# Optimization experiments

Hardware: AMD Instinct MI355X
Metric: run time of the kernel (lower is better)

Reference implementation:

```python
import jax, jax.numpy as jnp
import numpy as np

N, E, G = 100000, 1600000, 1024
F_IN, D, C = 1, 32, 10

def _lin(key, fin, fout):
    return jax.random.normal(key, (fin, fout), jnp.float32) / np.sqrt(fin)

def setup_inputs() -> dict:
    key = jax.random.key(0)
    ks = jax.random.split(key, 32)
    inp = {}
    inp['x'] = jax.random.normal(ks[0], (N, F_IN), jnp.float32)
    inp['edge_index'] = jax.random.randint(ks[1], (2, E), 0, N)
    inp['batch'] = jnp.sort(jax.random.randint(ks[2], (N,), 0, G))
    inp['num_graphs'] = G
    # conv1: ResGatedGraphConv(F_IN -> D)
    inp['c1_Wk'] = _lin(ks[3], F_IN, D); inp['c1_bk'] = jnp.zeros((D,), jnp.float32)
    inp['c1_Wq'] = _lin(ks[4], F_IN, D); inp['c1_bq'] = jnp.zeros((D,), jnp.float32)
    inp['c1_Wv'] = _lin(ks[5], F_IN, D); inp['c1_bv'] = jnp.zeros((D,), jnp.float32)
    inp['c1_Wskip'] = _lin(ks[6], F_IN, D); inp['c1_b'] = jnp.zeros((D,), jnp.float32)
    # conv2: FiLMConv(D -> D), num_relations=1
    inp['c2_Wlin'] = _lin(ks[7], D, D)
    inp['c2_Wfilm'] = _lin(ks[8], D, 2 * D); inp['c2_bfilm'] = jnp.zeros((2 * D,), jnp.float32)
    inp['c2_Wls'] = _lin(ks[9], D, D)
    inp['c2_Wfs'] = _lin(ks[10], D, 2 * D)
    # conv3: ResGatedGraphConv(D -> D)
    inp['c3_Wk'] = _lin(ks[11], D, D); inp['c3_bk'] = jnp.zeros((D,), jnp.float32)
    inp['c3_Wq'] = _lin(ks[12], D, D); inp['c3_bq'] = jnp.zeros((D,), jnp.float32)
    inp['c3_Wv'] = _lin(ks[13], D, D); inp['c3_bv'] = jnp.zeros((D,), jnp.float32)
    inp['c3_Wskip'] = _lin(ks[14], D, D); inp['c3_b'] = jnp.zeros((D,), jnp.float32)
    # final classifier
    inp['lin_W'] = _lin(ks[15], D, C); inp['lin_b'] = jnp.zeros((C,), jnp.float32)
    return inp

def _res_gated(x, src, dst, Wk, bk, Wq, bq, Wv, bv, Wskip, b):
    # out_i = sum_{j->i} sigmoid(k_i + q_j) * v_j + W_skip x_i + b
    k = x @ Wk + bk
    q = x @ Wq + bq
    v = x @ Wv + bv
    msg = jax.nn.sigmoid(k[dst] + q[src]) * v[src]  # [E, D]
    agg = jax.ops.segment_sum(msg, dst, num_segments=x.shape[0])
    return agg + x @ Wskip + b

def _film(x, src, dst, Wlin, Wfilm, bfilm, Wls, Wfs):
    # skip path: relu(gamma_skip * (W_skip x) + beta_skip)
    bg_s = x @ Wfs                       # [N, 2D]
    beta_s, gamma_s = jnp.split(bg_s, 2, axis=-1)
    out = jax.nn.relu(gamma_s * (x @ Wls) + beta_s)
    # message path: relu(gamma_i * (W x_j) + beta_i), mean aggregation
    bg = x @ Wfilm + bfilm
    beta, gamma = jnp.split(bg, 2, axis=-1)
    xl = x @ Wlin
    msg = jax.nn.relu(gamma[dst] * xl[src] + beta[dst])  # [E, D]
    sums = jax.ops.segment_sum(msg, dst, num_segments=x.shape[0])
    cnt = jax.ops.segment_sum(jnp.ones((dst.shape[0], 1), x.dtype), dst, num_segments=x.shape[0])
    return out + sums / jnp.maximum(cnt, 1.0)

def reference(x, edge_index, batch, num_graphs,
              c1_Wk, c1_bk, c1_Wq, c1_bq, c1_Wv, c1_bv, c1_Wskip, c1_b,
              c2_Wlin, c2_Wfilm, c2_bfilm, c2_Wls, c2_Wfs,
              c3_Wk, c3_bk, c3_Wq, c3_bq, c3_Wv, c3_bv, c3_Wskip, c3_b,
              lin_W, lin_b):
    src, dst = edge_index[0], edge_index[1]
    h = _res_gated(x, src, dst, c1_Wk, c1_bk, c1_Wq, c1_bq, c1_Wv, c1_bv, c1_Wskip, c1_b)
    h = jax.nn.relu(h)
    h = _film(h, src, dst, c2_Wlin, c2_Wfilm, c2_bfilm, c2_Wls, c2_Wfs)
    h = jax.nn.relu(h)
    h = _res_gated(h, src, dst, c3_Wk, c3_bk, c3_Wq, c3_bq, c3_Wv, c3_bv, c3_Wskip, c3_b)
    # global mean pool over graphs
    sums = jax.ops.segment_sum(h, batch, num_segments=num_graphs)
    cnt = jax.ops.segment_sum(jnp.ones((h.shape[0], 1), h.dtype), batch, num_segments=num_graphs)
    g = sums / jnp.maximum(cnt, 1.0)
    # dropout is identity in eval mode
    return g @ lin_W + lin_b
```

## Files before the change

kernel.cpp:

```cpp
#include <hip/hip_runtime.h>

#define N_NODES 100000
#define N_EDGES 1600000
#define N_GRAPH 1024
#define NB      196
#define BCAP    10240
#define PEPT    16

typedef unsigned short u16;
typedef unsigned int   u32;

__device__ __forceinline__ u16 f2bf(float f) {
    u32 u = __float_as_uint(f);
    u += 0x7FFFu + ((u >> 16) & 1u);
    return (u16)(u >> 16);
}
__device__ __forceinline__ float bf2f(u16 h) { return __uint_as_float(((u32)h) << 16); }
__device__ __forceinline__ float rcpf(float x) { return __builtin_amdgcn_rcpf(x); }

__global__ __launch_bounds__(256) void k_partition(const int* __restrict__ ei,
                                                   int* __restrict__ gcnt,
                                                   int* __restrict__ bucketed)
{
    __shared__ int lcnt[NB], gbase[NB], lcur[NB];
    int t = threadIdx.x;
    for (int i = t; i < NB; i += 256) { lcnt[i] = 0; lcur[i] = 0; }
    __syncthreads();

    int ebase = blockIdx.x * (256 * PEPT);
    int pk[PEPT], bk[PEPT];
#pragma unroll
    for (int r = 0; r < PEPT; r++) {
        int e = ebase + r * 256 + t;
        if (e < N_EDGES) {
            int d = ei[N_EDGES + e];
            int s = ei[e];
            int b = d >> 9;
            bk[r] = b;
            pk[r] = ((d & 511) << 17) | s;
            atomicAdd(&lcnt[b], 1);
        } else bk[r] = -1;
    }
    __syncthreads();
    for (int i = t; i < NB; i += 256) gbase[i] = atomicAdd(&gcnt[i], lcnt[i]);
    __syncthreads();
#pragma unroll
    for (int r = 0; r < PEPT; r++) {
        if (bk[r] >= 0) {
            int b = bk[r];
            int pos = gbase[b] + atomicAdd(&lcur[b], 1);
            bucketed[b * BCAP + pos] = pk[r];
        }
    }
}

__global__ __launch_bounds__(256) void k_bscan(const int* __restrict__ gcnt,
                                               int* __restrict__ base)
{
    __shared__ int s[256];
    int t = threadIdx.x;
    int v = (t < NB) ? gcnt[t] : 0;
    s[t] = v;
    __syncthreads();
#pragma unroll
    for (int off = 1; off < 256; off <<= 1) {
        int u = (t >= off) ? s[t - off] : 0;
        __syncthreads();
        s[t] += u;
        __syncthreads();
    }
    base[t] = s[t] - v;
}

__global__ __launch_bounds__(512) void k_place(const int* __restrict__ bucketed,
                                               const int* __restrict__ gcnt,
                                               const int* __restrict__ base,
                                               int* __restrict__ csr,
                                               int* __restrict__ starts,
                                               int* __restrict__ cnt)
{
    __shared__ int scnt[512], sexc[512], scur[512];
    int b = blockIdx.x, t = threadIdx.x;
    int ecnt = gcnt[b];
    int ebase = base[b];
    const int* bp = bucketed + b * BCAP;

    scnt[t] = 0; scur[t] = 0;
    __syncthreads();
    for (int e = t; e < ecnt; e += 512) atomicAdd(&scnt[bp[e] >> 17], 1);
    __syncthreads();
    int v = scnt[t];
    sexc[t] = v;
    __syncthreads();
#pragma unroll
    for (int off = 1; off < 512; off <<= 1) {
        int u = (t >= off) ? sexc[t - off] : 0;
        __syncthreads();
        sexc[t] += u;
        __syncthreads();
    }
    int excl = sexc[t] - v;
    __syncthreads();
    sexc[t] = excl;
    __syncthreads();

    int node = b * 512 + t;
    if (node < N_NODES) { starts[node] = ebase + excl; cnt[node] = v; }

    for (int e = t; e < ecnt; e += 512) {
        int p = bp[e];
        int ld = p >> 17;
        int pos = ebase + sexc[ld] + atomicAdd(&scur[ld], 1);
        csr[pos] = p & 0x1FFFF;
    }
}

__global__ __launch_bounds__(256) void k_gstart(const int* __restrict__ batch,
                                                int* __restrict__ gstart)
{
    int g = blockIdx.x * 256 + threadIdx.x;
    if (g > N_GRAPH) return;
    int lo = 0, hi = N_NODES;
    while (lo < hi) {
        int mid = (lo + hi) >> 1;
        if (batch[mid] < g) lo = mid + 1; else hi = mid;
    }
    gstart[g] = lo;
}

#define EDGE1(XS, ACC) {                                                     \
    ACC.x += fmaf(XS, wv.x, bv4.x) *                                         \
             rcpf(fmaf(ek.x, __expf(-fmaf(XS, wq.x, bq4.x)), 1.0f));         \
    ACC.y += fmaf(XS, wv.y, bv4.y) *                                         \
             rcpf(fmaf(ek.y, __expf(-fmaf(XS, wq.y, bq4.y)), 1.0f));         \
    ACC.z += fmaf(XS, wv.z, bv4.z) *                                         \
             rcpf(fmaf(ek.z, __expf(-fmaf(XS, wq.z, bq4.z)), 1.0f));         \
    ACC.w += fmaf(XS, wv.w, bv4.w) *                                         \
             rcpf(fmaf(ek.w, __expf(-fmaf(XS, wq.w, bq4.w)), 1.0f)); }

__global__ __launch_bounds__(256) void k_gath1(
    const float* __restrict__ x, const int* __restrict__ csr_src,
    const int* __restrict__ starts, const int* __restrict__ cnt,
    const float* __restrict__ Wk, const float* __restrict__ bk,
    const float* __restrict__ Wq, const float* __restrict__ bq,
    const float* __restrict__ Wv, const float* __restrict__ bv,
    const float* __restrict__ Wskip, const float* __restrict__ b,
    float* __restrict__ h1)
{
    int tid = blockIdx.x * 256 + threadIdx.x;
    int i = tid >> 3, l = tid & 7;

    float xd = x[i];
    float4 wk = ((const float4*)Wk)[l], bk4 = ((const float4*)bk)[l];
    float4 wq = ((const float4*)Wq)[l], bq4 = ((const float4*)bq)[l];
    float4 wv = ((const float4*)Wv)[l], bv4 = ((const float4*)bv)[l];
    float4 ek;
    ek.x = __expf(-fmaf(xd, wk.x, bk4.x));
    ek.y = __expf(-fmaf(xd, wk.y, bk4.y));
    ek.z = __expf(-fmaf(xd, wk.z, bk4.z));
    ek.w = __expf(-fmaf(xd, wk.w, bk4.w));

    int base = starts[i], deg = cnt[i];
    float4 a0 = make_float4(0.f, 0.f, 0.f, 0.f);
    float4 a1 = make_float4(0.f, 0.f, 0.f, 0.f);
    int e = 0;
    for (; e + 1 < deg; e += 2) {
        int s0 = csr_src[base + e];
        int s1 = csr_src[base + e + 1];
        float x0 = x[s0], x1 = x[s1];
        EDGE1(x0, a0) EDGE1(x1, a1)
    }
    if (e < deg) {
        float x0 = x[csr_src[base + e]];
        EDGE1(x0, a0)
    }
    float4 ws4 = ((const float4*)Wskip)[l];
    float4 bb4 = ((const float4*)b)[l];
    float4 o = make_float4(a0.x + a1.x + fmaf(xd, ws4.x, bb4.x),
                           a0.y + a1.y + fmaf(xd, ws4.y, bb4.y),
                           a0.z + a1.z + fmaf(xd, ws4.z, bb4.z),
                           a0.w + a1.w + fmaf(xd, ws4.w, bb4.w));
    ((float4*)(h1 + (size_t)i * 32))[l] = o;
}

__device__ __forceinline__ float4 dot4(const float* __restrict__ h,
                                       const float* __restrict__ Wcol, int stride)
{
    float4 a = make_float4(0.f, 0.f, 0.f, 0.f);
#pragma unroll
    for (int k = 0; k < 32; k++) {
        float4 w = *(const float4*)(Wcol + k * stride);
        float hk = h[k];
        a.x = fmaf(hk, w.x, a.x);
        a.y = fmaf(hk, w.y, a.y);
        a.z = fmaf(hk, w.z, a.z);
        a.w = fmaf(hk, w.w, a.w);
    }
    return a;
}

__global__ __launch_bounds__(256) void k_node2(
    const float* __restrict__ h1,
    const float* __restrict__ Wlin, const float* __restrict__ Wfilm,
    const float* __restrict__ bfilm, const float* __restrict__ Wls,
    const float* __restrict__ Wfs,
    u16* __restrict__ skip2b, u16* __restrict__ bg2b, u16* __restrict__ xlb)
{
    __shared__ float sWlin[1024], sWfilm[2048], sWls[1024], sWfs[2048];
    int t = threadIdx.x;
    for (int idx = t; idx < 1024; idx += 256) sWlin[idx] = Wlin[idx];
    for (int idx = t; idx < 2048; idx += 256) sWfilm[idx] = Wfilm[idx];
    for (int idx = t; idx < 1024; idx += 256) sWls[idx] = Wls[idx];
    for (int idx = t; idx < 2048; idx += 256) sWfs[idx] = Wfs[idx];
    __syncthreads();

    int tid = blockIdx.x * 256 + t;
    int i = tid >> 3, l = tid & 7;

    float h[32];
    const float4* hp = (const float4*)(h1 + (size_t)i * 32);
#pragma unroll
    for (int j = 0; j < 8; j++) {
        float4 v = hp[j];
        h[4 * j + 0] = fmaxf(v.x, 0.f);
        h[4 * j + 1] = fmaxf(v.y, 0.f);
        h[4 * j + 2] = fmaxf(v.z, 0.f);
        h[4 * j + 3] = fmaxf(v.w, 0.f);
    }

    float4 bs = dot4(h, sWfs + l * 4, 64);
    float4 gs = dot4(h, sWfs + 32 + l * 4, 64);
    float4 ls = dot4(h, sWls + l * 4, 32);
    ushort4 sku;
    sku.x = f2bf(fmaxf(fmaf(gs.x, ls.x, bs.x), 0.f));
    sku.y = f2bf(fmaxf(fmaf(gs.y, ls.y, bs.y), 0.f));
    sku.z = f2bf(fmaxf(fmaf(gs.z, ls.z, bs.z), 0.f));
    sku.w = f2bf(fmaxf(fmaf(gs.w, ls.w, bs.w), 0.f));
    ((ushort4*)skip2b)[(size_t)i * 8 + l] = sku;

    float4 bf0 = ((const float4*)bfilm)[l * 2];
    float4 bf1 = ((const float4*)bfilm)[l * 2 + 1];
    float4 f0 = dot4(h, sWfilm + l * 8, 64);
    float4 f1 = dot4(h, sWfilm + l * 8 + 4, 64);
    f0.x += bf0.x; f0.y += bf0.y; f0.z += bf0.z; f0.w += bf0.w;
    f1.x += bf1.x; f1.y += bf1.y; f1.z += bf1.z; f1.w += bf1.w;
    uint4 pk;
    pk.x = (u32)f2bf(f0.x) | ((u32)f2bf(f0.y) << 16);
    pk.y = (u32)f2bf(f0.z) | ((u32)f2bf(f0.w) << 16);
    pk.z = (u32)f2bf(f1.x) | ((u32)f2bf(f1.y) << 16);
    pk.w = (u32)f2bf(f1.z) | ((u32)f2bf(f1.w) << 16);
    ((uint4*)bg2b)[(size_t)i * 8 + l] = pk;

    float4 xo = dot4(h, sWlin + l * 4, 32);
    ushort4 xp;
    xp.x = f2bf(xo.x); xp.y = f2bf(xo.y); xp.z = f2bf(xo.z); xp.w = f2bf(xo.w);
    ((ushort4*)xlb)[(size_t)i * 8 + l] = xp;
}

#define EDGE_ACC2(U, ACC)                                   \
    ACC.x += fmaxf(fmaf(ga.x, bf2f(U.x), be.x), 0.f);       \
    ACC.y += fmaxf(fmaf(ga.y, bf2f(U.y), be.y), 0.f);       \
    ACC.z += fmaxf(fmaf(ga.z, bf2f(U.z), be.z), 0.f);       \
    ACC.w += fmaxf(fmaf(ga.w, bf2f(U.w), be.w), 0.f);

__global__ __launch_bounds__(256) void k_gath2(
    const int* __restrict__ csr_src, const int* __restrict__ starts,
    const int* __restrict__ cnt,
    const u16* __restrict__ bg2b, const u16* __restrict__ xlb,
    const u16* __restrict__ skip2b, float* __restrict__ h2)
{
    int tid = blockIdx.x * 256 + threadIdx.x;
    int i = tid >> 3, l = tid & 7;

    const u16* row = bg2b + (size_t)i * 64;
    ushort4 beu = *(const ushort4*)(row + l * 4);
    ushort4 gau = *(const ushort4*)(row + 32 + l * 4);
    float4 be = make_float4(bf2f(beu.x), bf2f(beu.y), bf2f(beu.z), bf2f(beu.w));
    float4 ga = make_float4(bf2f(gau.x), bf2f(gau.y), bf2f(gau.z), bf2f(gau.w));

    int base = starts[i], deg = cnt[i];
    const ushort4* xp = (const ushort4*)xlb;
    float4 a0 = make_float4(0.f, 0.f, 0.f, 0.f);
    float4 a1 = make_float4(0.f, 0.f, 0.f, 0.f);
    int e = 0;
    for (; e + 3 < deg; e += 4) {
        int s0 = csr_src[base + e];
        int s1 = csr_src[base + e + 1];
        int s2 = csr_src[base + e + 2];
        int s3 = csr_src[base + e + 3];
        ushort4 u0 = xp[(size_t)s0 * 8 + l];
        ushort4 u1 = xp[(size_t)s1 * 8 + l];
        ushort4 u2 = xp[(size_t)s2 * 8 + l];
        ushort4 u3 = xp[(size_t)s3 * 8 + l];
        EDGE_ACC2(u0, a0) EDGE_ACC2(u1, a1) EDGE_ACC2(u2, a0) EDGE_ACC2(u3, a1)
    }
    for (; e < deg; e++) {
        ushort4 u0 = xp[(size_t)csr_src[base + e] * 8 + l];
        EDGE_ACC2(u0, a0)
    }
    float inv = rcpf(fmaxf((float)deg, 1.0f));
    ushort4 sku = ((const ushort4*)skip2b)[(size_t)i * 8 + l];
    float4 o = make_float4(
        fmaxf(fmaf(a0.x + a1.x, inv, bf2f(sku.x)), 0.f),
        fmaxf(fmaf(a0.y + a1.y, inv, bf2f(sku.y)), 0.f),
        fmaxf(fmaf(a0.z + a1.z, inv, bf2f(sku.z)), 0.f),
        fmaxf(fmaf(a0.w + a1.w, inv, bf2f(sku.w)), 0.f));
    ((float4*)(h2 + (size_t)i * 32))[l] = o;
}

__global__ __launch_bounds__(256) void k_node3(
    const float* __restrict__ h2,
    const float* __restrict__ Wk, const float* __restrict__ bk,
    const float* __restrict__ Wq, const float* __restrict__ bq,
    const float* __restrict__ Wv, const float* __restrict__ bv,
    const float* __restrict__ Wskip, const float* __restrict__ b,
    u16* __restrict__ ek3b, u32* __restrict__ qvb, float* __restrict__ acc3)
{
    __shared__ float sWk[1024], sWq[1024], sWv[1024], sWs[1024];
    int t = threadIdx.x;
    for (int idx = t; idx < 1024; idx += 256) {
        sWk[idx] = Wk[idx];
        sWq[idx] = Wq[idx];
        sWv[idx] = Wv[idx];
        sWs[idx] = Wskip[idx];
    }
    __syncthreads();

    int tid = blockIdx.x * 256 + t;
    int i = tid >> 3, l = tid & 7;

    float h[32];
    const float4* hp = (const float4*)(h2 + (size_t)i * 32);
#pragma unroll
    for (int j = 0; j < 8; j++) {
        float4 v = hp[j];
        h[4 * j + 0] = v.x; h[4 * j + 1] = v.y;
        h[4 * j + 2] = v.z; h[4 * j + 3] = v.w;
    }

    float4 bk4 = ((const float4*)bk)[l];
    float4 bq4 = ((const float4*)bq)[l];
    float4 bv4 = ((const float4*)bv)[l];
    float4 bb4 = ((const float4*)b)[l];

    float4 kk = dot4(h, sWk + l * 4, 32);
    ushort4 eku;
    eku.x = f2bf(__expf(-(kk.x + bk4.x)));
    eku.y = f2bf(__expf(-(kk.y + bk4.y)));
    eku.z = f2bf(__expf(-(kk.z + bk4.z)));
    eku.w = f2bf(__expf(-(kk.w + bk4.w)));
    ((ushort4*)ek3b)[(size_t)i * 8 + l] = eku;

    float4 qq = dot4(h, sWq + l * 4, 32);
    float4 vv = dot4(h, sWv + l * 4, 32);
    float eq0 = __expf(-(qq.x + bq4.x));
    float eq1 = __expf(-(qq.y + bq4.y));
    float eq2 = __expf(-(qq.z + bq4.z));
    float eq3 = __expf(-(qq.w + bq4.w));
    vv.x += bv4.x; vv.y += bv4.y; vv.z += bv4.z; vv.w += bv4.w;

    uint4 pk;
    pk.x = (u32)f2bf(eq0) | ((u32)f2bf(eq1) << 16);
    pk.y = (u32)f2bf(eq2) | ((u32)f2bf(eq3) << 16);
    pk.z = (u32)f2bf(vv.x) | ((u32)f2bf(vv.y) << 16);
    pk.w = (u32)f2bf(vv.z) | ((u32)f2bf(vv.w) << 16);
    ((uint4*)qvb)[(size_t)i * 8 + l] = pk;

    float4 ss = dot4(h, sWs + l * 4, 32);
    ss.x += bb4.x; ss.y += bb4.y; ss.z += bb4.z; ss.w += bb4.w;
    ((float4*)(acc3 + (size_t)i * 32))[l] = ss;
}

#define EDGE_ACC(P, ACC)                                                        \
    ACC.x += bf2f((u16)(P.z)) * rcpf(fmaf(ek.x, bf2f((u16)(P.x)), 1.0f));       \
    ACC.y += bf2f((u16)(P.z >> 16)) * rcpf(fmaf(ek.y, bf2f((u16)(P.x >> 16)), 1.0f)); \
    ACC.z += bf2f((u16)(P.w)) * rcpf(fmaf(ek.z, bf2f((u16)(P.y)), 1.0f));       \
    ACC.w += bf2f((u16)(P.w >> 16)) * rcpf(fmaf(ek.w, bf2f((u16)(P.y >> 16)), 1.0f));

__global__ __launch_bounds__(256) void k_gath3p(
    const int* __restrict__ csr_src, const int* __restrict__ starts,
    const int* __restrict__ cnt,
    const u16* __restrict__ ek3b, const u32* __restrict__ qvb,
    const float* __restrict__ acc3, const int* __restrict__ batch,
    float* __restrict__ gsum)
{
    __shared__ float sg[8][32];
    int t = threadIdx.x;
    int tid = blockIdx.x * 256 + t;
    int i = tid >> 3, l = tid & 7;

    sg[t >> 5][t & 31] = 0.f;
    int gmin = batch[blockIdx.x * 32];
    __syncthreads();

    ushort4 eku = ((const ushort4*)ek3b)[(size_t)i * 8 + l];
    float4 ek = make_float4(bf2f(eku.x), bf2f(eku.y), bf2f(eku.z), bf2f(eku.w));
    int base = starts[i], deg = cnt[i];
    const uint4* qv = (const uint4*)qvb;
    float4 a0 = make_float4(0.f, 0.f, 0.f, 0.f);
    float4 a1 = make_float4(0.f, 0.f, 0.f, 0.f);
    int e = 0;
    for (; e + 3 < deg; e += 4) {
        int s0 = csr_src[base + e];
        int s1 = csr_src[base + e + 1];
        int s2 = csr_src[base + e + 2];
        int s3 = csr_src[base + e + 3];
        uint4 p0 = qv[(size_t)s0 * 8 + l];
        uint4 p1 = qv[(size_t)s1 * 8 + l];
        uint4 p2 = qv[(size_t)s2 * 8 + l];
        uint4 p3 = qv[(size_t)s3 * 8 + l];
        EDGE_ACC(p0, a0) EDGE_ACC(p1, a1) EDGE_ACC(p2, a0) EDGE_ACC(p3, a1)
    }
    for (; e < deg; e++) {
        uint4 p0 = qv[(size_t)csr_src[base + e] * 8 + l];
        EDGE_ACC(p0, a0)
    }
    float4 ss = ((const float4*)(acc3 + (size_t)i * 32))[l];
    float4 o = make_float4(ss.x + a0.x + a1.x, ss.y + a0.y + a1.y,
                           ss.z + a0.z + a1.z, ss.w + a0.w + a1.w);

    int g = batch[i];
    int slot = g - gmin;
    if (slot < 8) {
        atomicAdd(&sg[slot][l * 4 + 0], o.x);
        atomicAdd(&sg[slot][l * 4 + 1], o.y);
        atomicAdd(&sg[slot][l * 4 + 2], o.z);
        atomicAdd(&sg[slot][l * 4 + 3], o.w);
    } else {
        atomicAdd(&gsum[(size_t)g * 32 + l * 4 + 0], o.x);
        atomicAdd(&gsum[(size_t)g * 32 + l * 4 + 1], o.y);
        atomicAdd(&gsum[(size_t)g * 32 + l * 4 + 2], o.z);
        atomicAdd(&gsum[(size_t)g * 32 + l * 4 + 3], o.w);
    }
    __syncthreads();
    int slot2 = t >> 5, feat = t & 31;
    float v = sg[slot2][feat];
    int gout = gmin + slot2;
    if (v != 0.f && gout < N_GRAPH)
        atomicAdd(&gsum[(size_t)gout * 32 + feat], v);
}

__global__ __launch_bounds__(256) void k_final(
    const float* __restrict__ gsum, const int* __restrict__ gstart,
    const float* __restrict__ linW, const float* __restrict__ linb,
    float* __restrict__ out)
{
    int tid = blockIdx.x * 256 + threadIdx.x;
    if (tid >= N_GRAPH * 10) return;
    int g = tid / 10, c = tid % 10;
    float inv = rcpf(fmaxf((float)(gstart[g + 1] - gstart[g]), 1.0f));
    const float* gr = gsum + (size_t)g * 32;
    float a = 0.f;
#pragma unroll
    for (int k = 0; k < 32; k++) a = fmaf(gr[k], linW[k * 10 + c], a);
    out[tid] = fmaf(a, inv, linb[c]);
}

extern "C" void kernel_launch(void* const* d_in, const int* in_sizes, int n_in,
                              void* d_out, int out_size, void* d_ws, size_t ws_size,
                              hipStream_t stream)
{
    const float* x      = (const float*)d_in[0];
    const int*   ei     = (const int*)d_in[1];
    const int*   batch  = (const int*)d_in[2];
    const float* c1_Wk   = (const float*)d_in[4];
    const float* c1_bk   = (const float*)d_in[5];
    const float* c1_Wq   = (const float*)d_in[6];
    const float* c1_bq   = (const float*)d_in[7];
    const float* c1_Wv   = (const float*)d_in[8];
    const float* c1_bv   = (const float*)d_in[9];
    const float* c1_Wsk  = (const float*)d_in[10];
    const float* c1_b    = (const float*)d_in[11];
    const float* c2_Wlin = (const float*)d_in[12];
    const float* c2_Wfilm= (const float*)d_in[13];
    const float* c2_bfilm= (const float*)d_in[14];
    const float* c2_Wls  = (const float*)d_in[15];
    const float* c2_Wfs  = (const float*)d_in[16];
    const float* c3_Wk   = (const float*)d_in[17];
    const float* c3_bk   = (const float*)d_in[18];
    const float* c3_Wq   = (const float*)d_in[19];
    const float* c3_bq   = (const float*)d_in[20];
    const float* c3_Wv   = (const float*)d_in[21];
    const float* c3_bv   = (const float*)d_in[22];
    const float* c3_Wsk  = (const float*)d_in[23];
    const float* c3_b    = (const float*)d_in[24];
    const float* lin_W   = (const float*)d_in[25];
    const float* lin_b   = (const float*)d_in[26];
    float* out = (float*)d_out;

    const size_t N = N_NODES;

    int*   gcnt    = (int*)d_ws;
    float* gsum    = (float*)(gcnt + 256);
    int*   bbase   = (int*)(gsum + N_GRAPH * 32);
    int*   igstart = bbase + 256;
    int*   bucketed= igstart + 1056;
    int*   icsr    = bucketed + NB * BCAP;
    int*   istarts = icsr + N_EDGES;
    int*   icnt    = istarts + N;
    float* h1      = (float*)(icnt + N);
    u16*   skip2b  = (u16*)(h1 + N * 32);
    u16*   bg2b    = skip2b + N * 32;
    u16*   xlb     = bg2b + N * 64;
    float* acc3    = (float*)(xlb + N * 32);

    hipMemsetAsync(gcnt, 0, 256 * sizeof(int) + N_GRAPH * 32 * sizeof(float), stream);

    const int TB = 256;
    int gPart  = (N_EDGES + 256 * PEPT - 1) / (256 * PEPT);
    int gNode8 = (N_NODES * 8) / TB;
    int gFin   = (N_GRAPH * 10 + TB - 1) / TB;

    k_partition<<<gPart, TB, 0, stream>>>(ei, gcnt, bucketed);
    k_bscan<<<1, 256, 0, stream>>>(gcnt, bbase);
    k_place<<<NB, 512, 0, stream>>>(bucketed, gcnt, bbase, icsr, istarts, icnt);
    k_gstart<<<5, TB, 0, stream>>>(batch, igstart);

    k_gath1<<<gNode8, TB, 0, stream>>>(x, icsr, istarts, icnt,
                                       c1_Wk, c1_bk, c1_Wq, c1_bq,
                                       c1_Wv, c1_bv, c1_Wsk, c1_b, h1);
    k_node2<<<gNode8, TB, 0, stream>>>(h1, c2_Wlin, c2_Wfilm, c2_bfilm,
                                       c2_Wls, c2_Wfs, skip2b, bg2b, xlb);
    float* h2 = h1;
    k_gath2<<<gNode8, TB, 0, stream>>>(icsr, istarts, icnt, bg2b, xlb, skip2b, h2);
    u16* ek3b = skip2b;
    u32* qvb  = (u32*)bg2b;
    k_node3<<<gNode8, TB, 0, stream>>>(h2, c3_Wk, c3_bk, c3_Wq, c3_bq,
                                       c3_Wv, c3_bv, c3_Wsk, c3_b,
                                       ek3b, qvb, acc3);
    k_gath3p<<<gNode8, TB, 0, stream>>>(icsr, istarts, icnt, ek3b, qvb, acc3,
                                        batch, gsum);
    k_final<<<gFin, TB, 0, stream>>>(gsum, igstart, lin_W, lin_b, out);
}
```

Measured before the change: 304.5 us.

## Store intermediate node features in bf16, fold small kernels, deepen gather unrolls

Intermediate node activations (h1, h2, and the conv3 skip term) are now stored in bf16 instead of fp32, which halves their memory traffic between kernels. The bucket prefix scan moves inside k_place, and the graph-start binary search moves inside k_final, removing two tiny kernel launches. Edge loops in gath1 and gath2 are unrolled further to keep more loads in flight. The cost is lower precision in the stored activations, plus redundant scan work in every k_place block.

```diff
diff --git a/kernel.cpp b/kernel.cpp
--- a/kernel.cpp
+++ b/kernel.cpp
@@ -54,35 +54,28 @@
     }
 }
 
-__global__ __launch_bounds__(256) void k_bscan(const int* __restrict__ gcnt,
-                                               int* __restrict__ base)
-{
-    __shared__ int s[256];
-    int t = threadIdx.x;
-    int v = (t < NB) ? gcnt[t] : 0;
-    s[t] = v;
-    __syncthreads();
-#pragma unroll
-    for (int off = 1; off < 256; off <<= 1) {
-        int u = (t >= off) ? s[t - off] : 0;
-        __syncthreads();
-        s[t] += u;
-        __syncthreads();
-    }
-    base[t] = s[t] - v;
-}
-
 __global__ __launch_bounds__(512) void k_place(const int* __restrict__ bucketed,
                                                const int* __restrict__ gcnt,
-                                               const int* __restrict__ base,
                                                int* __restrict__ csr,
                                                int* __restrict__ starts,
                                                int* __restrict__ cnt)
 {
+    __shared__ int sb[256];
     __shared__ int scnt[512], sexc[512], scur[512];
     int b = blockIdx.x, t = threadIdx.x;
+
+    if (t < 256) sb[t] = (t < NB) ? gcnt[t] : 0;
+    __syncthreads();
+#pragma unroll
+    for (int off = 1; off < 256; off <<= 1) {
+        int u = 0;
+        if (t < 256 && t >= off) u = sb[t - off];
+        __syncthreads();
+        if (t < 256) sb[t] += u;
+        __syncthreads();
+    }
     int ecnt = gcnt[b];
-    int ebase = base[b];
+    int ebase = sb[b] - ecnt;
     const int* bp = bucketed + b * BCAP;
 
     scnt[t] = 0; scur[t] = 0;
@@ -113,19 +106,6 @@
         int pos = ebase + sexc[ld] + atomicAdd(&scur[ld], 1);
         csr[pos] = p & 0x1FFFF;
     }
-}
-
-__global__ __launch_bounds__(256) void k_gstart(const int* __restrict__ batch,
-                                                int* __restrict__ gstart)
-{
-    int g = blockIdx.x * 256 + threadIdx.x;
-    if (g > N_GRAPH) return;
-    int lo = 0, hi = N_NODES;
-    while (lo < hi) {
-        int mid = (lo + hi) >> 1;
-        if (batch[mid] < g) lo = mid + 1; else hi = mid;
-    }
-    gstart[g] = lo;
 }
 
 #define EDGE1(XS, ACC) {                                                     \
@@ -145,7 +125,7 @@
     const float* __restrict__ Wq, const float* __restrict__ bq,
     const float* __restrict__ Wv, const float* __restrict__ bv,
     const float* __restrict__ Wskip, const float* __restrict__ b,
-    float* __restrict__ h1)
+    u16* __restrict__ h1b)
 {
     int tid = blockIdx.x * 256 + threadIdx.x;
     int i = tid >> 3, l = tid & 7;
@@ -164,23 +144,26 @@
     float4 a0 = make_float4(0.f, 0.f, 0.f, 0.f);
     float4 a1 = make_float4(0.f, 0.f, 0.f, 0.f);
     int e = 0;
-    for (; e + 1 < deg; e += 2) {
+    for (; e + 3 < deg; e += 4) {
         int s0 = csr_src[base + e];
         int s1 = csr_src[base + e + 1];
-        float x0 = x[s0], x1 = x[s1];
-        EDGE1(x0, a0) EDGE1(x1, a1)
-    }
-    if (e < deg) {
+        int s2 = csr_src[base + e + 2];
+        int s3 = csr_src[base + e + 3];
+        float x0 = x[s0], x1 = x[s1], x2 = x[s2], x3 = x[s3];
+        EDGE1(x0, a0) EDGE1(x1, a1) EDGE1(x2, a0) EDGE1(x3, a1)
+    }
+    for (; e < deg; e++) {
         float x0 = x[csr_src[base + e]];
         EDGE1(x0, a0)
     }
     float4 ws4 = ((const float4*)Wskip)[l];
     float4 bb4 = ((const float4*)b)[l];
-    float4 o = make_float4(a0.x + a1.x + fmaf(xd, ws4.x, bb4.x),
-                           a0.y + a1.y + fmaf(xd, ws4.y, bb4.y),
-                           a0.z + a1.z + fmaf(xd, ws4.z, bb4.z),
-                           a0.w + a1.w + fmaf(xd, ws4.w, bb4.w));
-    ((float4*)(h1 + (size_t)i * 32))[l] = o;
+    ushort4 o;
+    o.x = f2bf(a0.x + a1.x + fmaf(xd, ws4.x, bb4.x));
+    o.y = f2bf(a0.y + a1.y + fmaf(xd, ws4.y, bb4.y));
+    o.z = f2bf(a0.z + a1.z + fmaf(xd, ws4.z, bb4.z));
+    o.w = f2bf(a0.w + a1.w + fmaf(xd, ws4.w, bb4.w));
+    ((ushort4*)h1b)[(size_t)i * 8 + l] = o;
 }
 
 __device__ __forceinline__ float4 dot4(const float* __restrict__ h,
@@ -199,8 +182,30 @@
     return a;
 }
 
+__device__ __forceinline__ void load_row_bf16(const u16* __restrict__ rowb,
+                                              size_t i, float* h, bool relu)
+{
+    const uint4* rp = (const uint4*)rowb + i * 4;
+#pragma unroll
+    for (int j = 0; j < 4; j++) {
+        uint4 q = rp[j];
+        float v0 = bf2f((u16)q.x), v1 = bf2f((u16)(q.x >> 16));
+        float v2 = bf2f((u16)q.y), v3 = bf2f((u16)(q.y >> 16));
+        float v4 = bf2f((u16)q.z), v5 = bf2f((u16)(q.z >> 16));
+        float v6 = bf2f((u16)q.w), v7 = bf2f((u16)(q.w >> 16));
+        if (relu) {
+            v0 = fmaxf(v0, 0.f); v1 = fmaxf(v1, 0.f);
+            v2 = fmaxf(v2, 0.f); v3 = fmaxf(v3, 0.f);
+            v4 = fmaxf(v4, 0.f); v5 = fmaxf(v5, 0.f);
+            v6 = fmaxf(v6, 0.f); v7 = fmaxf(v7, 0.f);
+        }
+        h[8 * j + 0] = v0; h[8 * j + 1] = v1; h[8 * j + 2] = v2; h[8 * j + 3] = v3;
+        h[8 * j + 4] = v4; h[8 * j + 5] = v5; h[8 * j + 6] = v6; h[8 * j + 7] = v7;
+    }
+}
+
 __global__ __launch_bounds__(256) void k_node2(
-    const float* __restrict__ h1,
+    const u16* __restrict__ h1b,
     const float* __restrict__ Wlin, const float* __restrict__ Wfilm,
     const float* __restrict__ bfilm, const float* __restrict__ Wls,
     const float* __restrict__ Wfs,
@@ -218,15 +223,7 @@
     int i = tid >> 3, l = tid & 7;
 
     float h[32];
-    const float4* hp = (const float4*)(h1 + (size_t)i * 32);
-#pragma unroll
-    for (int j = 0; j < 8; j++) {
-        float4 v = hp[j];
-        h[4 * j + 0] = fmaxf(v.x, 0.f);
-        h[4 * j + 1] = fmaxf(v.y, 0.f);
-        h[4 * j + 2] = fmaxf(v.z, 0.f);
-        h[4 * j + 3] = fmaxf(v.w, 0.f);
-    }
+    load_row_bf16(h1b, (size_t)i, h, true);
 
     float4 bs = dot4(h, sWfs + l * 4, 64);
     float4 gs = dot4(h, sWfs + 32 + l * 4, 64);
@@ -267,7 +264,7 @@
     const int* __restrict__ csr_src, const int* __restrict__ starts,
     const int* __restrict__ cnt,
     const u16* __restrict__ bg2b, const u16* __restrict__ xlb,
-    const u16* __restrict__ skip2b, float* __restrict__ h2)
+    const u16* __restrict__ skip2b, u16* __restrict__ h2b)
 {
     int tid = blockIdx.x * 256 + threadIdx.x;
     int i = tid >> 3, l = tid & 7;
@@ -283,16 +280,25 @@
     float4 a0 = make_float4(0.f, 0.f, 0.f, 0.f);
     float4 a1 = make_float4(0.f, 0.f, 0.f, 0.f);
     int e = 0;
-    for (; e + 3 < deg; e += 4) {
+    for (; e + 7 < deg; e += 8) {
         int s0 = csr_src[base + e];
         int s1 = csr_src[base + e + 1];
         int s2 = csr_src[base + e + 2];
         int s3 = csr_src[base + e + 3];
+        int s4 = csr_src[base + e + 4];
+        int s5 = csr_src[base + e + 5];
+        int s6 = csr_src[base + e + 6];
+        int s7 = csr_src[base + e + 7];
         ushort4 u0 = xp[(size_t)s0 * 8 + l];
         ushort4 u1 = xp[(size_t)s1 * 8 + l];
         ushort4 u2 = xp[(size_t)s2 * 8 + l];
         ushort4 u3 = xp[(size_t)s3 * 8 + l];
+        ushort4 u4 = xp[(size_t)s4 * 8 + l];
+        ushort4 u5 = xp[(size_t)s5 * 8 + l];
+        ushort4 u6 = xp[(size_t)s6 * 8 + l];
+        ushort4 u7 = xp[(size_t)s7 * 8 + l];
         EDGE_ACC2(u0, a0) EDGE_ACC2(u1, a1) EDGE_ACC2(u2, a0) EDGE_ACC2(u3, a1)
+        EDGE_ACC2(u4, a0) EDGE_ACC2(u5, a1) EDGE_ACC2(u6, a0) EDGE_ACC2(u7, a1)
     }
     for (; e < deg; e++) {
         ushort4 u0 = xp[(size_t)csr_src[base + e] * 8 + l];
@@ -300,21 +306,21 @@
     }
     float inv = rcpf(fmaxf((float)deg, 1.0f));
     ushort4 sku = ((const ushort4*)skip2b)[(size_t)i * 8 + l];
-    float4 o = make_float4(
-        fmaxf(fmaf(a0.x + a1.x, inv, bf2f(sku.x)), 0.f),
-        fmaxf(fmaf(a0.y + a1.y, inv, bf2f(sku.y)), 0.f),
-        fmaxf(fmaf(a0.z + a1.z, inv, bf2f(sku.z)), 0.f),
-        fmaxf(fmaf(a0.w + a1.w, inv, bf2f(sku.w)), 0.f));
-    ((float4*)(h2 + (size_t)i * 32))[l] = o;
+    ushort4 o;
+    o.x = f2bf(fmaxf(fmaf(a0.x + a1.x, inv, bf2f(sku.x)), 0.f));
+    o.y = f2bf(fmaxf(fmaf(a0.y + a1.y, inv, bf2f(sku.y)), 0.f));
+    o.z = f2bf(fmaxf(fmaf(a0.z + a1.z, inv, bf2f(sku.z)), 0.f));
+    o.w = f2bf(fmaxf(fmaf(a0.w + a1.w, inv, bf2f(sku.w)), 0.f));
+    ((ushort4*)h2b)[(size_t)i * 8 + l] = o;
 }
 
 __global__ __launch_bounds__(256) void k_node3(
-    const float* __restrict__ h2,
+    const u16* __restrict__ h2b,
     const float* __restrict__ Wk, const float* __restrict__ bk,
     const float* __restrict__ Wq, const float* __restrict__ bq,
     const float* __restrict__ Wv, const float* __restrict__ bv,
     const float* __restrict__ Wskip, const float* __restrict__ b,
-    u16* __restrict__ ek3b, u32* __restrict__ qvb, float* __restrict__ acc3)
+    u16* __restrict__ ek3b, u32* __restrict__ qvb, u16* __restrict__ acc3b)
 {
     __shared__ float sWk[1024], sWq[1024], sWv[1024], sWs[1024];
     int t = threadIdx.x;
@@ -330,13 +336,7 @@
     int i = tid >> 3, l = tid & 7;
 
     float h[32];
-    const float4* hp = (const float4*)(h2 + (size_t)i * 32);
-#pragma unroll
-    for (int j = 0; j < 8; j++) {
-        float4 v = hp[j];
-        h[4 * j + 0] = v.x; h[4 * j + 1] = v.y;
-        h[4 * j + 2] = v.z; h[4 * j + 3] = v.w;
-    }
+    load_row_bf16(h2b, (size_t)i, h, false);
 
     float4 bk4 = ((const float4*)bk)[l];
     float4 bq4 = ((const float4*)bq)[l];
@@ -367,8 +367,12 @@
     ((uint4*)qvb)[(size_t)i * 8 + l] = pk;
 
     float4 ss = dot4(h, sWs + l * 4, 32);
-    ss.x += bb4.x; ss.y += bb4.y; ss.z += bb4.z; ss.w += bb4.w;
-    ((float4*)(acc3 + (size_t)i * 32))[l] = ss;
+    ushort4 so;
+    so.x = f2bf(ss.x + bb4.x);
+    so.y = f2bf(ss.y + bb4.y);
+    so.z = f2bf(ss.z + bb4.z);
+    so.w = f2bf(ss.w + bb4.w);
+    ((ushort4*)acc3b)[(size_t)i * 8 + l] = so;
 }
 
 #define EDGE_ACC(P, ACC)                                                        \
@@ -381,7 +385,7 @@
     const int* __restrict__ csr_src, const int* __restrict__ starts,
     const int* __restrict__ cnt,
     const u16* __restrict__ ek3b, const u32* __restrict__ qvb,
-    const float* __restrict__ acc3, const int* __restrict__ batch,
+    const u16* __restrict__ acc3b, const int* __restrict__ batch,
     float* __restrict__ gsum)
 {
     __shared__ float sg[8][32];
@@ -415,9 +419,9 @@
         uint4 p0 = qv[(size_t)csr_src[base + e] * 8 + l];
         EDGE_ACC(p0, a0)
     }
-    float4 ss = ((const float4*)(acc3 + (size_t)i * 32))[l];
-    float4 o = make_float4(ss.x + a0.x + a1.x, ss.y + a0.y + a1.y,
-                           ss.z + a0.z + a1.z, ss.w + a0.w + a1.w);
+    ushort4 sku = ((const ushort4*)acc3b)[(size_t)i * 8 + l];
+    float4 o = make_float4(bf2f(sku.x) + a0.x + a1.x, bf2f(sku.y) + a0.y + a1.y,
+                           bf2f(sku.z) + a0.z + a1.z, bf2f(sku.w) + a0.w + a1.w);
 
     int g = batch[i];
     int slot = g - gmin;
@@ -440,15 +444,27 @@
         atomicAdd(&gsum[(size_t)gout * 32 + feat], v);
 }
 
+__device__ __forceinline__ int lower_bound(const int* __restrict__ a, int key)
+{
+    int lo = 0, hi = N_NODES;
+    while (lo < hi) {
+        int mid = (lo + hi) >> 1;
+        if (a[mid] < key) lo = mid + 1; else hi = mid;
+    }
+    return lo;
+}
+
 __global__ __launch_bounds__(256) void k_final(
-    const float* __restrict__ gsum, const int* __restrict__ gstart,
+    const float* __restrict__ gsum, const int* __restrict__ batch,
     const float* __restrict__ linW, const float* __restrict__ linb,
     float* __restrict__ out)
 {
     int tid = blockIdx.x * 256 + threadIdx.x;
     if (tid >= N_GRAPH * 10) return;
     int g = tid / 10, c = tid % 10;
-    float inv = rcpf(fmaxf((float)(gstart[g + 1] - gstart[g]), 1.0f));
+    int s = lower_bound(batch, g);
+    int e = lower_bound(batch, g + 1);
+    float inv = rcpf(fmaxf((float)(e - s), 1.0f));
     const float* gr = gsum + (size_t)g * 32;
     float a = 0.f;
 #pragma unroll
@@ -492,17 +508,15 @@
 
     int*   gcnt    = (int*)d_ws;
     float* gsum    = (float*)(gcnt + 256);
-    int*   bbase   = (int*)(gsum + N_GRAPH * 32);
-    int*   igstart = bbase + 256;
-    int*   bucketed= igstart + 1056;
+    int*   bucketed= (int*)(gsum + N_GRAPH * 32);
     int*   icsr    = bucketed + NB * BCAP;
     int*   istarts = icsr + N_EDGES;
     int*   icnt    = istarts + N;
-    float* h1      = (float*)(icnt + N);
-    u16*   skip2b  = (u16*)(h1 + N * 32);
+    u16*   h1b     = (u16*)(icnt + N);
+    u16*   skip2b  = h1b + N * 32;
     u16*   bg2b    = skip2b + N * 32;
     u16*   xlb     = bg2b + N * 64;
-    float* acc3    = (float*)(xlb + N * 32);
+    u16*   acc3b   = xlb + N * 32;
 
     hipMemsetAsync(gcnt, 0, 256 * sizeof(int) + N_GRAPH * 32 * sizeof(float), stream);
 
@@ -512,23 +526,21 @@
     int gFin   = (N_GRAPH * 10 + TB - 1) / TB;
 
     k_partition<<<gPart, TB, 0, stream>>>(ei, gcnt, bucketed);
-    k_bscan<<<1, 256, 0, stream>>>(gcnt, bbase);
-    k_place<<<NB, 512, 0, stream>>>(bucketed, gcnt, bbase, icsr, istarts, icnt);
-    k_gstart<<<5, TB, 0, stream>>>(batch, igstart);
+    k_place<<<NB, 512, 0, stream>>>(bucketed, gcnt, icsr, istarts, icnt);
 
     k_gath1<<<gNode8, TB, 0, stream>>>(x, icsr, istarts, icnt,
                                        c1_Wk, c1_bk, c1_Wq, c1_bq,
-                                       c1_Wv, c1_bv, c1_Wsk, c1_b, h1);
-    k_node2<<<gNode8, TB, 0, stream>>>(h1, c2_Wlin, c2_Wfilm, c2_bfilm,
+                                       c1_Wv, c1_bv, c1_Wsk, c1_b, h1b);
+    k_node2<<<gNode8, TB, 0, stream>>>(h1b, c2_Wlin, c2_Wfilm, c2_bfilm,
                                        c2_Wls, c2_Wfs, skip2b, bg2b, xlb);
-    float* h2 = h1;
-    k_gath2<<<gNode8, TB, 0, stream>>>(icsr, istarts, icnt, bg2b, xlb, skip2b, h2);
+    u16* h2b = h1b;
+    k_gath2<<<gNode8, TB, 0, stream>>>(icsr, istarts, icnt, bg2b, xlb, skip2b, h2b);
     u16* ek3b = skip2b;
     u32* qvb  = (u32*)bg2b;
-    k_node3<<<gNode8, TB, 0, stream>>>(h2, c3_Wk, c3_bk, c3_Wq, c3_bq,
+    k_node3<<<gNode8, TB, 0, stream>>>(h2b, c3_Wk, c3_bk, c3_Wq, c3_bq,
                                        c3_Wv, c3_bv, c3_Wsk, c3_b,
-                                       ek3b, qvb, acc3);
-    k_gath3p<<<gNode8, TB, 0, stream>>>(icsr, istarts, icnt, ek3b, qvb, acc3,
+                                       ek3b, qvb, acc3b);
+    k_gath3p<<<gNode8, TB, 0, stream>>>(icsr, istarts, icnt, ek3b, qvb, acc3b,
                                         batch, gsum);
-    k_final<<<gFin, TB, 0, stream>>>(gsum, igstart, lin_W, lin_b, out);
-}
+    k_final<<<gFin, TB, 0, stream>>>(gsum, batch, lin_W, lin_b, out);
+}
```

Result: slower. 311.2 us (+2.2%).
